# Kernel tuning notes

Measured on AMD Instinct MI355X. Metric: run time of the kernel, lower is better.

Reference implementation:

```python
import jax, jax.numpy as jnp
import numpy as np

BATCH = 32768
TEXT_DIM = 384
HIDDEN = 256
NUM_LAYERS = 4
NUM_VERTS = 12
K_NN = 6


def _build_template():
    """Icosphere vertices (12, normalized) and row-normalized kNN adjacency (12,12)."""
    phi = (1.0 + 5.0 ** 0.5) / 2.0
    v = np.array([
        [-1, phi, 0], [1, phi, 0], [-1, -phi, 0], [1, -phi, 0],
        [0, -1, phi], [0, 1, phi], [0, -1, -phi], [0, 1, -phi],
        [phi, 0, -1], [phi, 0, 1], [-phi, 0, -1], [-phi, 0, 1],
    ], dtype=np.float32)
    v = v / np.linalg.norm(v, axis=1, keepdims=True)
    dist = np.linalg.norm(v[:, None, :] - v[None, :, :], axis=-1)  # (12,12)
    # k+1 smallest per row; index 0 is self (distance 0), skip it
    idx = np.argsort(dist, axis=1, kind='stable')[:, 1:K_NN + 1]
    adj = np.zeros((NUM_VERTS, NUM_VERTS), dtype=np.float32)
    rows = np.repeat(np.arange(NUM_VERTS), K_NN)
    adj[rows, idx.reshape(-1)] = 1.0
    adj = adj / (adj.sum(axis=1, keepdims=True) + 1e-6)
    return jnp.asarray(v), jnp.asarray(adj)


def setup_inputs() -> dict:
    key = jax.random.key(0)
    ks = jax.random.split(key, 8)
    template, adjacency = _build_template()
    scale = 0.02
    return {
        "text_emb": jax.random.normal(ks[0], (BATCH, TEXT_DIM), dtype=jnp.float32),
        "W_text": jax.random.normal(ks[1], (TEXT_DIM, HIDDEN), dtype=jnp.float32) * scale,
        "b_text": jnp.zeros((HIDDEN,), dtype=jnp.float32),
        "W_gnn": jax.random.normal(ks[2], (NUM_LAYERS, HIDDEN, HIDDEN), dtype=jnp.float32) * scale,
        "b_gnn": jnp.zeros((NUM_LAYERS, HIDDEN), dtype=jnp.float32),
        "W_out": jax.random.normal(ks[3], (HIDDEN, 3), dtype=jnp.float32) * scale,
        "b_out": jnp.zeros((3,), dtype=jnp.float32),
        "adjacency": adjacency,   # (12,12) buffer
        "template": template,     # (12,3) buffer
    }


def reference(text_emb, W_text, b_text, W_gnn, b_gnn, W_out, b_out, adjacency, template):
    # text projection -> broadcast to all nodes
    tf = text_emb @ W_text + b_text                       # (B, H)
    B = text_emb.shape[0]
    h = jnp.broadcast_to(tf[:, None, :], (B, NUM_VERTS, HIDDEN))
    # GNN layers: aggregate (shared adjacency across batch), project, relu
    for l in range(NUM_LAYERS):
        agg = jnp.einsum('nm,bmd->bnd', adjacency, h)     # (B, 12, H)
        h = jax.nn.relu(agg @ W_gnn[l] + b_gnn[l])
    displacements = h @ W_out + b_out                     # (B, 12, 3)
    return template[None, :, :] + displacements
```

## Files before the change

kernel.cpp:

```cpp
#include <hip/hip_runtime.h>
#include <stdint.h>

#define TD      384
#define HID     256

typedef __bf16 bf16;
typedef __attribute__((ext_vector_type(8))) __bf16 bf16x8;
typedef __attribute__((ext_vector_type(4))) float f32x4;

union FragU { uint4 u; bf16x8 f; };
union PackU { uint4 u; bf16 v[8]; };

__device__ inline f32x4 mfma16(bf16x8 a, bf16x8 b, f32x4 c) {
  return __builtin_amdgcn_mfma_f32_16x16x32_bf16(a, b, c, 0, 0, 0);
}

__global__ __launch_bounds__(256) void prep_wf(
    const float* __restrict__ W_text, const float* __restrict__ b_text,
    const float* __restrict__ W_gnn, const float* __restrict__ b_gnn,
    float* __restrict__ wf, float* __restrict__ bfv)
{
  int n = threadIdx.x;
  int k = blockIdx.x;
  const float* g0 = W_gnn;
  if (k < TD) {
    const float* trow = W_text + (size_t)k * HID;
    float a0 = 0.f, a1 = 0.f, a2 = 0.f, a3 = 0.f;
    for (int j = 0; j < HID; j += 4) {
      a0 += trow[j]     * g0[(j    ) * HID + n];
      a1 += trow[j + 1] * g0[(j + 1) * HID + n];
      a2 += trow[j + 2] * g0[(j + 2) * HID + n];
      a3 += trow[j + 3] * g0[(j + 3) * HID + n];
    }
    wf[(size_t)k * HID + n] = (a0 + a1) + (a2 + a3);
  } else {
    float a0 = 0.f, a1 = 0.f, a2 = 0.f, a3 = 0.f;
    for (int j = 0; j < HID; j += 4) {
      a0 += b_text[j]     * g0[(j    ) * HID + n];
      a1 += b_text[j + 1] * g0[(j + 1) * HID + n];
      a2 += b_text[j + 2] * g0[(j + 2) * HID + n];
      a3 += b_text[j + 3] * g0[(j + 3) * HID + n];
    }
    bfv[n] = (a0 + a1) + (a2 + a3) + b_gnn[n];
  }
}

__global__ __launch_bounds__(256) void prep_pack(
    const float* __restrict__ wf, const float* __restrict__ W_gnn,
    const float* __restrict__ W_out,
    bf16* __restrict__ wt_f, bf16* __restrict__ wt_g, float* __restrict__ wot)
{
  int bid = blockIdx.x, tid = threadIdx.x;
  if (bid < 48) {
    int idx = bid * 256 + tid;
    int cc = idx & 15, c = idx >> 4;
    int n16 = c / 48, oct = c - n16 * 48;
    int n = n16 * 16 + cc;
    PackU pk;
    #pragma unroll
    for (int j = 0; j < 8; j++) pk.v[j] = (bf16)wf[(oct * 8 + j) * HID + n];
    *(uint4*)(wt_f + idx * 8) = pk.u;
  } else if (bid < 144) {
    int idx = (bid - 48) * 256 + tid;
    int cc = idx & 15, c = idx >> 4;
    int l = c >> 9, c2 = c & 511;
    int oct = c2 & 31;
    int n = (c2 >> 5) * 16 + cc;
    const float* base = W_gnn + (size_t)(l + 1) * HID * HID;
    PackU pk;
    #pragma unroll
    for (int j = 0; j < 8; j++) pk.v[j] = (bf16)base[(oct * 8 + j) * HID + n];
    *(uint4*)(wt_g + idx * 8) = pk.u;
  } else {
    for (int t = tid; t < 3 * HID; t += 256) {
      int comp = t >> 8, k = t & 255;
      wot[comp * HID + k] = W_out[k * 3 + comp];
    }
  }
}

__global__ __launch_bounds__(256, 3) void mesh_kernel(
    const float* __restrict__ text,
    const bf16* __restrict__ wt_f,
    const bf16* __restrict__ wt_g,
    const float* __restrict__ b_f,
    const float* __restrict__ b_gnn,
    const float* __restrict__ wot,
    const float* __restrict__ b_out,
    const float* __restrict__ tmpl,
    float* __restrict__ out)
{
  __shared__ __align__(16) unsigned char smem[49920];
  unsigned char* Tbuf = smem;
  float* dispBuf = (float*)(smem + 49152);

  const int tid  = threadIdx.x;
  const int lane = tid & 63;
  const int w    = tid >> 6;
  const int cc   = lane & 15;
  const int qq   = lane >> 4;
  const int rowbase = blockIdx.x * 64;

  f32x4 acc[4][4];

  auto zero_acc = [&]() {
    f32x4 z = {0.f, 0.f, 0.f, 0.f};
    #pragma unroll
    for (int mt = 0; mt < 4; mt++)
      #pragma unroll
      for (int nt = 0; nt < 4; nt++) acc[mt][nt] = z;
  };

  auto loadA = [&](const unsigned char* src, int rowB, int ks, bf16x8* A) {
    #pragma unroll
    for (int mt = 0; mt < 4; mt++) {
      int m = mt * 16 + cc;
      FragU fu;
      fu.u = *(const uint4*)(src + m * rowB + (((ks * 4 + qq) ^ (m & 7)) * 16));
      A[mt] = fu.f;
    }
  };

  auto loadB = [&](const char* wb, int K8, int ks, bf16x8* B) {
    #pragma unroll
    for (int nt = 0; nt < 4; nt++) {
      FragU fu;
      fu.u = *(const uint4*)(wb + (size_t)(nt * K8 + ks * 4) * 256);
      B[nt] = fu.f;
    }
  };

  auto epilogue = [&](const float* bias_ptr, bool relu) {
    float bias4[4];
    #pragma unroll
    for (int nt = 0; nt < 4; nt++) bias4[nt] = bias_ptr[w * 64 + nt * 16 + cc];
    #pragma unroll
    for (int mt = 0; mt < 4; mt++) {
      #pragma unroll
      for (int nt = 0; nt < 4; nt++) {
        int col = w * 64 + nt * 16 + cc;
        #pragma unroll
        for (int r = 0; r < 4; r++) {
          int m = mt * 16 + qq * 4 + r;
          float v = acc[mt][nt][r] + bias4[nt];
          if (relu) v = fmaxf(v, 0.f);
          *(bf16*)(Tbuf + m * 512 + ((col >> 3) ^ (m & 7)) * 16 + (col & 7) * 2) = (bf16)v;
        }
      }
    }
  };

  const float* tbase = text + (size_t)rowbase * TD;
  float4 pf[6];

  auto stageLoad = [&](int c) {
    #pragma unroll
    for (int i = 0; i < 3; i++) {
      int id = i * 256 + tid;
      int m = id / 12, ol = id - m * 12;
      const float4* p = (const float4*)(tbase + m * TD + (c * 12 + ol) * 8);
      pf[2 * i]     = p[0];
      pf[2 * i + 1] = p[1];
    }
  };
  auto stageWrite = [&](int c) {
    #pragma unroll
    for (int i = 0; i < 3; i++) {
      int id = i * 256 + tid;
      int m = id / 12, ol = id - m * 12;
      int o = c * 12 + ol;
      float4 x = pf[2 * i], y = pf[2 * i + 1];
      PackU pk;
      pk.v[0]=(bf16)x.x; pk.v[1]=(bf16)x.y; pk.v[2]=(bf16)x.z; pk.v[3]=(bf16)x.w;
      pk.v[4]=(bf16)y.x; pk.v[5]=(bf16)y.y; pk.v[6]=(bf16)y.z; pk.v[7]=(bf16)y.w;
      *(uint4*)(Tbuf + m * 768 + ((o ^ (m & 7)) * 16)) = pk.u;
    }
  };

  zero_acc();
  stageLoad(0);
  stageWrite(0);
  __syncthreads();

  const char* wbf = (const char*)wt_f + (size_t)(w * 4 * 48 + qq) * 256 + cc * 16;
  {
    bf16x8 B[4], Bn[4];
    loadB(wbf, 48, 0, B);
    for (int c = 0; c < 4; c++) {
      if (c < 3) stageLoad(c + 1);
      #pragma unroll
      for (int k2 = 0; k2 < 3; k2++) {
        int ks = c * 3 + k2;
        if (ks < 11) loadB(wbf, 48, ks + 1, Bn);
        bf16x8 A[4];
        loadA(Tbuf, 768, ks, A);
        #pragma unroll
        for (int mt = 0; mt < 4; mt++)
          #pragma unroll
          for (int nt = 0; nt < 4; nt++)
            acc[mt][nt] = mfma16(A[mt], B[nt], acc[mt][nt]);
        if (ks < 11) {
          #pragma unroll
          for (int t = 0; t < 4; t++) B[t] = Bn[t];
        }
      }
      if (c < 3) stageWrite(c + 1);
      __syncthreads();
    }
  }
  epilogue(b_f, true);
  __syncthreads();

  for (int l = 0; l < 3; l++) {
    const char* wb = (const char*)wt_g + (size_t)l * HID * HID * 2
                   + (size_t)(w * 4 * 32 + qq) * 256 + cc * 16;
    zero_acc();
    bf16x8 A[4], B[4], An[4], Bn[4];
    loadB(wb, 32, 0, B);
    loadA(Tbuf, 512, 0, A);
    #pragma unroll
    for (int ks = 0; ks < 8; ks++) {
      if (ks < 7) {
        loadB(wb, 32, ks + 1, Bn);
        loadA(Tbuf, 512, ks + 1, An);
      }
      #pragma unroll
      for (int mt = 0; mt < 4; mt++)
        #pragma unroll
        for (int nt = 0; nt < 4; nt++)
          acc[mt][nt] = mfma16(A[mt], B[nt], acc[mt][nt]);
      if (ks < 7) {
        #pragma unroll
        for (int t = 0; t < 4; t++) { A[t] = An[t]; B[t] = Bn[t]; }
      }
    }
    __syncthreads();
    epilogue(b_gnn + (l + 1) * HID, true);
    __syncthreads();
  }

  if (tid < 192) {
    int comp = tid >> 6;
    int r = tid & 63;
    const float4* wrow = (const float4*)(wot + comp * HID);
    float s = 0.f;
    #pragma unroll 4
    for (int o = 0; o < 32; o++) {
      FragU fu; fu.u = *(const uint4*)(Tbuf + r * 512 + ((o ^ (r & 7)) * 16));
      float4 w0 = wrow[2 * o], w1 = wrow[2 * o + 1];
      s += (float)fu.f[0]*w0.x + (float)fu.f[1]*w0.y + (float)fu.f[2]*w0.z + (float)fu.f[3]*w0.w;
      s += (float)fu.f[4]*w1.x + (float)fu.f[5]*w1.y + (float)fu.f[6]*w1.z + (float)fu.f[7]*w1.w;
    }
    dispBuf[r * 3 + comp] = s + b_out[comp];
  }
  __syncthreads();

  #pragma unroll
  for (int ii = 0; ii < 9; ii++) {
    int i = ii * 256 + tid;
    int row = i / 36;
    int j = i - row * 36;
    out[(size_t)rowbase * 36 + i] = tmpl[j] + dispBuf[row * 3 + j % 3];
  }
}

extern "C" void kernel_launch(void* const* d_in, const int* in_sizes, int n_in,
                              void* d_out, int out_size, void* d_ws, size_t ws_size,
                              hipStream_t stream) {
  const float* text   = (const float*)d_in[0];
  const float* W_text = (const float*)d_in[1];
  const float* b_text = (const float*)d_in[2];
  const float* W_gnn  = (const float*)d_in[3];
  const float* b_gnn  = (const float*)d_in[4];
  const float* W_out  = (const float*)d_in[5];
  const float* b_out  = (const float*)d_in[6];
  const float* tmpl   = (const float*)d_in[8];
  float* outp = (float*)d_out;

  float* wf   = (float*)d_ws;
  float* bfv  = wf + TD * HID;
  float* wot  = bfv + HID;
  bf16* wt_f  = (bf16*)(wot + 3 * HID);
  bf16* wt_g  = wt_f + TD * HID;

  prep_wf<<<TD + 1, 256, 0, stream>>>(W_text, b_text, W_gnn, b_gnn, wf, bfv);
  prep_pack<<<145, 256, 0, stream>>>(wf, W_gnn, W_out, wt_f, wt_g, wot);
  mesh_kernel<<<32768 / 64, 256, 0, stream>>>(text, wt_f, wt_g, bfv, b_gnn,
                                              wot, b_out, tmpl, outp);
}
```

Before: 151.1 us.

## Split mesh kernel work across 8 waves with row halves per wave

The block grows from 256 to 512 threads. Each wave now computes a 32-row by 64-column tile instead of 64x64, which halves the accumulator registers and allows more waves in flight. The text staging pipeline changes from four register-prefetched chunks to two halves written directly into LDS, with the second half overlapping the first half's MFMAs. This trades per-wave B-fragment reuse (each B is now loaded by two waves) for occupancy and latency hiding, and removes the register prefetch buffer.

```diff
diff --git a/kernel.cpp b/kernel.cpp
--- a/kernel.cpp
+++ b/kernel.cpp
@@ -79,7 +79,7 @@
   }
 }
 
-__global__ __launch_bounds__(256, 3) void mesh_kernel(
+__global__ __launch_bounds__(512, 4) void mesh_kernel(
     const float* __restrict__ text,
     const bf16* __restrict__ wt_f,
     const bf16* __restrict__ wt_g,
@@ -97,26 +97,28 @@
   const int tid  = threadIdx.x;
   const int lane = tid & 63;
   const int w    = tid >> 6;
+  const int cs   = w & 3;
+  const int rh   = w >> 2;
   const int cc   = lane & 15;
   const int qq   = lane >> 4;
   const int rowbase = blockIdx.x * 64;
 
-  f32x4 acc[4][4];
+  f32x4 acc[2][4];
 
   auto zero_acc = [&]() {
     f32x4 z = {0.f, 0.f, 0.f, 0.f};
     #pragma unroll
-    for (int mt = 0; mt < 4; mt++)
+    for (int mt = 0; mt < 2; mt++)
       #pragma unroll
       for (int nt = 0; nt < 4; nt++) acc[mt][nt] = z;
   };
 
-  auto loadA = [&](const unsigned char* src, int rowB, int ks, bf16x8* A) {
-    #pragma unroll
-    for (int mt = 0; mt < 4; mt++) {
-      int m = mt * 16 + cc;
+  auto loadA = [&](int rowB, int ks, bf16x8* A) {
+    #pragma unroll
+    for (int mt = 0; mt < 2; mt++) {
+      int m = rh * 32 + mt * 16 + cc;
       FragU fu;
-      fu.u = *(const uint4*)(src + m * rowB + (((ks * 4 + qq) ^ (m & 7)) * 16));
+      fu.u = *(const uint4*)(Tbuf + m * rowB + (((ks * 4 + qq) ^ (m & 7)) * 16));
       A[mt] = fu.f;
     }
   };
@@ -133,15 +135,15 @@
   auto epilogue = [&](const float* bias_ptr, bool relu) {
     float bias4[4];
     #pragma unroll
-    for (int nt = 0; nt < 4; nt++) bias4[nt] = bias_ptr[w * 64 + nt * 16 + cc];
-    #pragma unroll
-    for (int mt = 0; mt < 4; mt++) {
+    for (int nt = 0; nt < 4; nt++) bias4[nt] = bias_ptr[cs * 64 + nt * 16 + cc];
+    #pragma unroll
+    for (int mt = 0; mt < 2; mt++) {
       #pragma unroll
       for (int nt = 0; nt < 4; nt++) {
-        int col = w * 64 + nt * 16 + cc;
+        int col = cs * 64 + nt * 16 + cc;
         #pragma unroll
         for (int r = 0; r < 4; r++) {
-          int m = mt * 16 + qq * 4 + r;
+          int m = rh * 32 + mt * 16 + qq * 4 + r;
           float v = acc[mt][nt][r] + bias4[nt];
           if (relu) v = fmaxf(v, 0.f);
           *(bf16*)(Tbuf + m * 512 + ((col >> 3) ^ (m & 7)) * 16 + (col & 7) * 2) = (bf16)v;
@@ -151,25 +153,14 @@
   };
 
   const float* tbase = text + (size_t)rowbase * TD;
-  float4 pf[6];
-
-  auto stageLoad = [&](int c) {
+  auto stageHalf = [&](int half) {
     #pragma unroll
     for (int i = 0; i < 3; i++) {
-      int id = i * 256 + tid;
-      int m = id / 12, ol = id - m * 12;
-      const float4* p = (const float4*)(tbase + m * TD + (c * 12 + ol) * 8);
-      pf[2 * i]     = p[0];
-      pf[2 * i + 1] = p[1];
-    }
-  };
-  auto stageWrite = [&](int c) {
-    #pragma unroll
-    for (int i = 0; i < 3; i++) {
-      int id = i * 256 + tid;
-      int m = id / 12, ol = id - m * 12;
-      int o = c * 12 + ol;
-      float4 x = pf[2 * i], y = pf[2 * i + 1];
+      int id = i * 512 + tid;
+      int m = id / 24, ol = id - m * 24;
+      int o = half * 24 + ol;
+      const float4* p = (const float4*)(tbase + m * TD + o * 8);
+      float4 x = p[0], y = p[1];
       PackU pk;
       pk.v[0]=(bf16)x.x; pk.v[1]=(bf16)x.y; pk.v[2]=(bf16)x.z; pk.v[3]=(bf16)x.w;
       pk.v[4]=(bf16)y.x; pk.v[5]=(bf16)y.y; pk.v[6]=(bf16)y.z; pk.v[7]=(bf16)y.w;
@@ -177,61 +168,73 @@
     }
   };
 
+  stageHalf(0);
+  __syncthreads();
+  stageHalf(1);
   zero_acc();
-  stageLoad(0);
-  stageWrite(0);
-  __syncthreads();
-
-  const char* wbf = (const char*)wt_f + (size_t)(w * 4 * 48 + qq) * 256 + cc * 16;
+  const char* wbf = (const char*)wt_f + (size_t)(cs * 4 * 48 + qq) * 256 + cc * 16;
   {
-    bf16x8 B[4], Bn[4];
+    bf16x8 A[2], B[4], An[2], Bn[4];
     loadB(wbf, 48, 0, B);
-    for (int c = 0; c < 4; c++) {
-      if (c < 3) stageLoad(c + 1);
-      #pragma unroll
-      for (int k2 = 0; k2 < 3; k2++) {
-        int ks = c * 3 + k2;
-        if (ks < 11) loadB(wbf, 48, ks + 1, Bn);
-        bf16x8 A[4];
-        loadA(Tbuf, 768, ks, A);
-        #pragma unroll
-        for (int mt = 0; mt < 4; mt++)
-          #pragma unroll
-          for (int nt = 0; nt < 4; nt++)
-            acc[mt][nt] = mfma16(A[mt], B[nt], acc[mt][nt]);
-        if (ks < 11) {
-          #pragma unroll
-          for (int t = 0; t < 4; t++) B[t] = Bn[t];
-        }
-      }
-      if (c < 3) stageWrite(c + 1);
-      __syncthreads();
-    }
-  }
+    loadA(768, 0, A);
+    #pragma unroll
+    for (int ks = 0; ks < 6; ks++) {
+      if (ks < 5) { loadB(wbf, 48, ks + 1, Bn); loadA(768, ks + 1, An); }
+      #pragma unroll
+      for (int mt = 0; mt < 2; mt++)
+        #pragma unroll
+        for (int nt = 0; nt < 4; nt++)
+          acc[mt][nt] = mfma16(A[mt], B[nt], acc[mt][nt]);
+      if (ks < 5) {
+        #pragma unroll
+        for (int t = 0; t < 2; t++) A[t] = An[t];
+        #pragma unroll
+        for (int t = 0; t < 4; t++) B[t] = Bn[t];
+      }
+    }
+    __syncthreads();
+    loadB(wbf, 48, 6, B);
+    loadA(768, 6, A);
+    #pragma unroll
+    for (int ks = 6; ks < 12; ks++) {
+      if (ks < 11) { loadB(wbf, 48, ks + 1, Bn); loadA(768, ks + 1, An); }
+      #pragma unroll
+      for (int mt = 0; mt < 2; mt++)
+        #pragma unroll
+        for (int nt = 0; nt < 4; nt++)
+          acc[mt][nt] = mfma16(A[mt], B[nt], acc[mt][nt]);
+      if (ks < 11) {
+        #pragma unroll
+        for (int t = 0; t < 2; t++) A[t] = An[t];
+        #pragma unroll
+        for (int t = 0; t < 4; t++) B[t] = Bn[t];
+      }
+    }
+  }
+  __syncthreads();
   epilogue(b_f, true);
   __syncthreads();
 
   for (int l = 0; l < 3; l++) {
     const char* wb = (const char*)wt_g + (size_t)l * HID * HID * 2
-                   + (size_t)(w * 4 * 32 + qq) * 256 + cc * 16;
+                   + (size_t)(cs * 4 * 32 + qq) * 256 + cc * 16;
     zero_acc();
-    bf16x8 A[4], B[4], An[4], Bn[4];
+    bf16x8 A[2], B[4], An[2], Bn[4];
     loadB(wb, 32, 0, B);
-    loadA(Tbuf, 512, 0, A);
+    loadA(512, 0, A);
     #pragma unroll
     for (int ks = 0; ks < 8; ks++) {
-      if (ks < 7) {
-        loadB(wb, 32, ks + 1, Bn);
-        loadA(Tbuf, 512, ks + 1, An);
-      }
-      #pragma unroll
-      for (int mt = 0; mt < 4; mt++)
+      if (ks < 7) { loadB(wb, 32, ks + 1, Bn); loadA(512, ks + 1, An); }
+      #pragma unroll
+      for (int mt = 0; mt < 2; mt++)
         #pragma unroll
         for (int nt = 0; nt < 4; nt++)
           acc[mt][nt] = mfma16(A[mt], B[nt], acc[mt][nt]);
       if (ks < 7) {
         #pragma unroll
-        for (int t = 0; t < 4; t++) { A[t] = An[t]; B[t] = Bn[t]; }
+        for (int t = 0; t < 2; t++) A[t] = An[t];
+        #pragma unroll
+        for (int t = 0; t < 4; t++) B[t] = Bn[t];
       }
     }
     __syncthreads();
@@ -256,11 +259,13 @@
   __syncthreads();
 
   #pragma unroll
-  for (int ii = 0; ii < 9; ii++) {
-    int i = ii * 256 + tid;
-    int row = i / 36;
-    int j = i - row * 36;
-    out[(size_t)rowbase * 36 + i] = tmpl[j] + dispBuf[row * 3 + j % 3];
+  for (int ii = 0; ii < 5; ii++) {
+    int i = ii * 512 + tid;
+    if (i < 2304) {
+      int row = i / 36;
+      int j = i - row * 36;
+      out[(size_t)rowbase * 36 + i] = tmpl[j] + dispBuf[row * 3 + j % 3];
+    }
   }
 }
 
@@ -285,6 +290,6 @@
 
   prep_wf<<<TD + 1, 256, 0, stream>>>(W_text, b_text, W_gnn, b_gnn, wf, bfv);
   prep_pack<<<145, 256, 0, stream>>>(wf, W_gnn, W_out, wt_f, wt_g, wot);
-  mesh_kernel<<<32768 / 64, 256, 0, stream>>>(text, wt_f, wt_g, bfv, b_gnn,
+  mesh_kernel<<<32768 / 64, 512, 0, stream>>>(text, wt_f, wt_g, bfv, b_gnn,
                                               wot, b_out, tmpl, outp);
 }
```

Result: faster. 144.2 us (-4.5%).
